# Kernel tuning notes

Measured on AMD Instinct MI355X. Metric: run time of the kernel, lower is better.

## Reference

```python
import jax, jax.numpy as jnp
import numpy as np

B = 2048          # env batch
N = 32            # num_svgd_particles
D = 6             # act_dim
OBS = 17          # obs_dim
H = 256           # q1 hidden width
STEPS = 10        # num_svgd_steps
LR = 0.1          # svgd_lr
LIMIT = 1.0       # act_limit
LOG_NP1 = np.float32(np.log(N + 1.0))


def setup_inputs() -> dict:
    key = jax.random.key(0)
    ks = jax.random.split(key, 6)
    obs = jax.random.normal(ks[0], (B * N, OBS), dtype=jnp.float32)
    a = jax.random.normal(ks[1], (B * N, D), dtype=jnp.float32)
    W1 = jax.random.normal(ks[2], (OBS + D, H), dtype=jnp.float32) / np.float32(np.sqrt(OBS + D))
    b1 = jnp.zeros((H,), dtype=jnp.float32)
    W2 = jax.random.normal(ks[3], (H, H), dtype=jnp.float32) / np.float32(np.sqrt(H))
    b2 = jnp.zeros((H,), dtype=jnp.float32)
    W3 = jax.random.normal(ks[4], (H, 1), dtype=jnp.float32) / np.float32(np.sqrt(H))
    b3 = jnp.zeros((1,), dtype=jnp.float32)
    return {"obs": obs, "a": a, "W1": W1, "b1": b1, "W2": W2, "b2": b2, "W3": W3, "b3": b3}


def q1(obs, X, W1, b1, W2, b2, W3, b3):
    # standard SAC critic: Q(s, a) = MLP(concat(s, a))
    h = jax.nn.relu(jnp.concatenate([obs, X], axis=-1) @ W1 + b1)
    h = jax.nn.relu(h @ W2 + b2)
    return (h @ W3 + b3).squeeze(-1)


def rbf(X):
    # X: (B, N, D); input_2 = X.detach() in the original
    Xd = jax.lax.stop_gradient(X)
    diff = X[:, :, None, :] - Xd[:, None, :, :]          # (B, N, N, D)
    dist_sq = jnp.sum(diff * diff, axis=-1)              # (B, N, N)
    nn = N * N
    # torch.median returns the LOWER of the two middle values for even counts
    med = jnp.sort(jax.lax.stop_gradient(dist_sq).reshape(-1, nn), axis=1)[:, (nn - 1) // 2]
    h = med / (2.0 * LOG_NP1)                            # bandwidth^2 (sigma^2 = h)
    gamma = 1.0 / (1e-8 + 2.0 * h)                       # (B,)
    gamma = gamma[:, None, None]                         # (B, 1, 1)
    kappa = jnp.exp(-gamma * dist_sq)                    # (B, N, N)
    kappa_grad = -2.0 * (diff * gamma[..., None]) * kappa[..., None]  # (B, N, N, D)
    return kappa, diff, gamma, kappa_grad


def reference(obs, a, W1, b1, W2, b2, W3, b3):
    score_fn = jax.grad(lambda Xf: q1(obs, Xf, W1, b1, W2, b2, W3, b3).sum())
    logp = jnp.zeros((B, N), dtype=jnp.float32)

    for _ in range(STEPS):
        score = score_fn(a)                              # (B*N, D)
        X = a.reshape(B, N, D)
        s = score.reshape(B, N, D)
        K_XX, K_diff, K_gamma, K_grad = rbf(X)
        Kd = jax.lax.stop_gradient(K_XX)
        phi = (jnp.einsum('bij,bjd->bid', Kd, s) - K_grad.sum(axis=2)) / N  # (B, N, D)
        line_4 = (K_grad * s[:, None, :, :]).sum(-1).mean(-1)               # (B, N)
        line_5 = -2.0 * K_gamma[:, :, 0] * (
            (-K_grad * K_diff).sum(-1) - D * K_XX
        ).mean(-1)                                                          # (B, N)
        logp = logp - LR * (line_4 + line_5)
        a = jnp.clip(a + LR * phi.reshape(B * N, D), -LIMIT, LIMIT)
        a = jax.lax.stop_gradient(a)

    return a, logp
```

## Files before the change

### kernel.cpp

```cpp
#include <hip/hip_runtime.h>
#include <hip/hip_bf16.h>

#define NB 2048
#define NP 32
#define ND 6
#define NOBS 17
#define NH 256
#define NSTEPS 10
#define C_LR 0.1f
#define C_LIM 1.0f
#define C_LOGNP1 3.4965075614664802f

typedef __bf16 bf16x8 __attribute__((ext_vector_type(8)));
typedef float  f32x4  __attribute__((ext_vector_type(4)));

#define MFMA(a, b, c) __builtin_amdgcn_mfma_f32_16x16x32_bf16(a, b, c, 0, 0, 0)

static __device__ __forceinline__ unsigned short f2bf(float f) {
    union { float f; unsigned u; } c; c.f = f;
    const unsigned r = c.u + 0x7fffu + ((c.u >> 16) & 1u);
    return (unsigned short)(r >> 16);
}

static __device__ __forceinline__ int colpf(int n) {
    return ((n >> 5) << 11) + (((n >> 3) & 3) << 7) + (n & 7);
}

__global__ void prep_swizzle(const float* __restrict__ W1, const float* __restrict__ W2,
                             unsigned short* __restrict__ ws) {
    const int g = blockIdx.x * 256 + threadIdx.x;
    unsigned short v[8];
    if (g < 8192) {
        const int l = g & 63, fid = g >> 6;
        const int kt = fid >> 4, nt = fid & 15;
        const int row0 = kt * 32 + (l >> 4) * 8;
        const int col  = nt * 16 + (l & 15);
#pragma unroll
        for (int j = 0; j < 8; ++j) v[j] = f2bf(W2[(row0 + j) * NH + col]);
        ushort4* dst = (ushort4*)(ws + (size_t)g * 8);
        dst[0] = make_ushort4(v[0], v[1], v[2], v[3]);
        dst[1] = make_ushort4(v[4], v[5], v[6], v[7]);
    } else if (g < 16384) {
        const int e = g - 8192;
        const int l = e & 63, fid = e >> 6;
        const int kt = fid >> 4, nt = fid & 15;
        const int row  = nt * 16 + (l & 15);
        const int col0 = kt * 32 + (l >> 4) * 8;
#pragma unroll
        for (int j = 0; j < 8; ++j) v[j] = f2bf(W2[row * NH + col0 + j]);
        ushort4* dst = (ushort4*)(ws + 65536 + (size_t)e * 8);
        dst[0] = make_ushort4(v[0], v[1], v[2], v[3]);
        dst[1] = make_ushort4(v[4], v[5], v[6], v[7]);
    } else if (g < 16896) {
        const int e = g - 16384;
        const int l = e & 63, kt = e >> 6;
        const int n  = l & 15;
        const int k0 = kt * 32 + (l >> 4) * 8;
#pragma unroll
        for (int j = 0; j < 8; ++j)
            v[j] = (n < ND) ? f2bf(W1[(NOBS + n) * NH + k0 + j]) : (unsigned short)0;
        ushort4* dst = (ushort4*)(ws + 131072 + (size_t)e * 8);
        dst[0] = make_ushort4(v[0], v[1], v[2], v[3]);
        dst[1] = make_ushort4(v[4], v[5], v[6], v[7]);
    } else if (g < 17920) {
        const int e = g - 16896;
        const int l = e & 63, nt = e >> 6;
        const int col = nt * 16 + (l & 15);
        const int r0  = (l >> 4) * 8;
#pragma unroll
        for (int j = 0; j < 8; ++j)
            v[j] = (r0 + j < NOBS + ND) ? f2bf(W1[(r0 + j) * NH + col]) : (unsigned short)0;
        ushort4* dst = (ushort4*)(ws + 135168 + (size_t)e * 8);
        dst[0] = make_ushort4(v[0], v[1], v[2], v[3]);
        dst[1] = make_ushort4(v[4], v[5], v[6], v[7]);
    }
}

__global__ __launch_bounds__(256, 4)
void svgd_kernel(const float* __restrict__ obs, const float* __restrict__ a_in,
                 const float* __restrict__ W1, const float* __restrict__ b1,
                 const float* __restrict__ W2, const float* __restrict__ b2,
                 const float* __restrict__ W3, const unsigned short* __restrict__ ws,
                 float* __restrict__ out)
{
    __shared__ __attribute__((aligned(16))) unsigned short hA[64 * NH];
    __shared__ float Xs[2][384];
    __shared__ float sc_[512];
    __shared__ float med_s[2];

    const int t    = threadIdx.x;
    const int bb   = blockIdx.x;
    const int lane = t & 63;
    const int wid  = t >> 6;
    const int w4   = wid * 4;
    const int quad = lane >> 4;
    const int ln15 = lane & 15;
    const int qo = t >> 7, iao = (t & 127) >> 2, jgo = t & 3;

    const unsigned short* gW2f = ws;
    const unsigned short* gW2b = ws + 65536;
    const unsigned short* gW1p = ws + 131072;
    const unsigned short* gW1f = ws + 135168;

    {
        float* scr = (float*)hA;
        const float* obs_g = obs + (size_t)bb * 1088;
        for (int p = t; p < 1088; p += 256) scr[p] = obs_g[p];
        const float* a_g = a_in + (size_t)bb * 384;
        for (int p = t; p < 384; p += 256) Xs[0][p] = a_g[p];
    }
    __syncthreads();
    bf16x8 a0[4];
    {
        const float* scr = (const float*)hA;
#pragma unroll
        for (int m = 0; m < 4; ++m) {
            const int s = m * 16 + ln15;
#pragma unroll
            for (int j = 0; j < 8; ++j) {
                const int k = quad * 8 + j;
                float v = 0.0f;
                if (k < NOBS) v = scr[s * NOBS + k];
                else if (k < NOBS + ND) v = Xs[0][s * 6 + (k - NOBS)];
                a0[m][j] = (__bf16)v;
            }
        }
    }
    __syncthreads();

    float b1r[4], b2r[4]; unsigned short w3u[4];
#pragma unroll
    for (int q = 0; q < 4; ++q) {
        const int n = (w4 + q) * 16 + ln15;
        b1r[q] = b1[n]; b2r[q] = b2[n]; w3u[q] = f2bf(W3[n]);
    }

    float logp_r = 0.0f;
    int cur = 0;
    const f32x4 zv = {0.f, 0.f, 0.f, 0.f};

    for (int step = 0; step < NSTEPS; ++step) {
        unsigned long long mask1 = 0ull;
        {
            bf16x8 w1B[4];
#pragma unroll
            for (int q = 0; q < 4; ++q)
                w1B[q] = *(const bf16x8*)(gW1f + ((w4 + q) * 64 + lane) * 8);
            f32x4 acc0[4][4];
#pragma unroll
            for (int m = 0; m < 4; ++m)
#pragma unroll
                for (int q = 0; q < 4; ++q) acc0[m][q] = MFMA(a0[m], w1B[q], zv);
#pragma unroll
            for (int q = 0; q < 4; ++q) {
                const int cp = colpf((w4 + q) * 16 + ln15);
#pragma unroll
                for (int m = 0; m < 4; ++m)
#pragma unroll
                    for (int reg = 0; reg < 4; ++reg) {
                        const float hv = acc0[m][q][reg] + b1r[q];
                        const int idx = cp + m * 512 + (quad * 4 + reg) * 8;
                        if (hv > 0.f) {
                            mask1 |= 1ull << (q * 16 + m * 4 + reg);
                            hA[idx] = f2bf(hv);
                        } else hA[idx] = 0;
                    }
            }
        }
        __syncthreads();

        {
            f32x4 acc[4][4];
#pragma unroll
            for (int m = 0; m < 4; ++m)
#pragma unroll
                for (int q = 0; q < 4; ++q) acc[m][q] = zv;
#pragma unroll 2
            for (int kt = 0; kt < 8; ++kt) {
                bf16x8 a[4];
#pragma unroll
                for (int m = 0; m < 4; ++m)
                    a[m] = *(const bf16x8*)&hA[(kt * 4 + m) * 512 + lane * 8];
#pragma unroll
                for (int q = 0; q < 4; ++q) {
                    const bf16x8 bf = *(const bf16x8*)(gW2f + ((kt * 16 + w4 + q) * 64 + lane) * 8);
#pragma unroll
                    for (int m = 0; m < 4; ++m) acc[m][q] = MFMA(a[m], bf, acc[m][q]);
                }
            }
            __syncthreads();
#pragma unroll
            for (int q = 0; q < 4; ++q) {
                const int cp = colpf((w4 + q) * 16 + ln15);
                const float b2v = b2r[q];
                const unsigned short w3v = w3u[q];
#pragma unroll
                for (int m = 0; m < 4; ++m)
#pragma unroll
                    for (int reg = 0; reg < 4; ++reg) {
                        const int idx = cp + m * 512 + (quad * 4 + reg) * 8;
                        hA[idx] = (acc[m][q][reg] + b2v > 0.f) ? w3v : (unsigned short)0;
                    }
            }
        }
        __syncthreads();

        {
            f32x4 acc2[4][4];
#pragma unroll
            for (int m = 0; m < 4; ++m)
#pragma unroll
                for (int q = 0; q < 4; ++q) acc2[m][q] = zv;
#pragma unroll 2
            for (int kt = 0; kt < 8; ++kt) {
                bf16x8 a[4];
#pragma unroll
                for (int m = 0; m < 4; ++m)
                    a[m] = *(const bf16x8*)&hA[(kt * 4 + m) * 512 + lane * 8];
#pragma unroll
                for (int q = 0; q < 4; ++q) {
                    const bf16x8 bf = *(const bf16x8*)(gW2b + ((kt * 16 + w4 + q) * 64 + lane) * 8);
#pragma unroll
                    for (int m = 0; m < 4; ++m) acc2[m][q] = MFMA(a[m], bf, acc2[m][q]);
                }
            }
            __syncthreads();
#pragma unroll
            for (int q = 0; q < 4; ++q) {
                const int cp = colpf((w4 + q) * 16 + ln15);
#pragma unroll
                for (int m = 0; m < 4; ++m)
#pragma unroll
                    for (int reg = 0; reg < 4; ++reg) {
                        const int idx = cp + m * 512 + (quad * 4 + reg) * 8;
                        hA[idx] = ((mask1 >> (q * 16 + m * 4 + reg)) & 1ull)
                                      ? f2bf(acc2[m][q][reg]) : (unsigned short)0;
                    }
            }
        }
        __syncthreads();

        if (wid >= 2) {
            const int mb = (wid - 2) * 2;
            f32x4 sa[2] = {zv, zv};
#pragma unroll
            for (int kt = 0; kt < 8; ++kt) {
                const bf16x8 bw = *(const bf16x8*)(gW1p + (kt * 64 + lane) * 8);
#pragma unroll
                for (int mm = 0; mm < 2; ++mm) {
                    const bf16x8 a = *(const bf16x8*)&hA[(kt * 4 + mb + mm) * 512 + lane * 8];
                    sa[mm] = MFMA(a, bw, sa[mm]);
                }
            }
            if (ln15 < ND) {
#pragma unroll
                for (int mm = 0; mm < 2; ++mm)
#pragma unroll
                    for (int reg = 0; reg < 4; ++reg)
                        sc_[((mb + mm) * 16 + quad * 4 + reg) * 8 + ln15] = sa[mm][reg];
            }
        } else {
            const float* Xc = &Xs[cur][wid * 192];
            unsigned u[8];
#pragma unroll
            for (int r = 0; r < 8; ++r) {
                const int e = lane + 64 * r;
                if (e < 496) {
                    int i = (int)((63.0f - sqrtf(3969.0f - 8.0f * (float)e)) * 0.5f);
                    while (i * (63 - i) / 2 > e) --i;
                    while ((i + 1) * (62 - i) / 2 <= e) ++i;
                    const int j = i + 1 + (e - i * (63 - i) / 2);
                    float s = 0.f;
#pragma unroll
                    for (int d = 0; d < ND; ++d) {
                        const float df = Xc[i * 6 + d] - Xc[j * 6 + d];
                        s += df * df;
                    }
                    u[r] = __float_as_uint(s);
                } else u[r] = 0x7f800000u;
            }
            unsigned P = 0u;
            for (int bit = 30; bit >= 0; --bit) {
                const unsigned Q = P | (1u << bit);
                int c = 0;
#pragma unroll
                for (int r = 0; r < 8; ++r)
                    c += __popcll(__ballot(u[r] < Q));
                if (c <= 239) P = Q;
            }
            if (lane == 0) med_s[wid] = __uint_as_float(P);
        }
        __syncthreads();

        {
            const int nxt = cur ^ 1;
            const float gam = 1.0f / (1e-8f + med_s[qo] / C_LOGNP1);
            const float* Xc = &Xs[cur][qo * 192];
            float xi[6];
#pragma unroll
            for (int d = 0; d < ND; ++d) xi[d] = Xc[iao * 6 + d];
            float w[8] = {0, 0, 0, 0, 0, 0, 0, 0};
#pragma unroll
            for (int jj = 0; jj < 8; ++jj) {
                const int j = jgo * 8 + jj;
                float df6[6], sj6[6];
                float dsv = 0.f, dot = 0.f;
#pragma unroll
                for (int d = 0; d < ND; ++d) {
                    df6[d] = xi[d] - Xc[j * 6 + d];
                    sj6[d] = sc_[(qo * 32 + j) * 8 + d];
                    dsv += df6[d] * df6[d];
                    dot += df6[d] * sj6[d];
                }
                const float kap = __expf(-gam * dsv);
                const float tg = 2.0f * gam * kap;
#pragma unroll
                for (int d = 0; d < ND; ++d) w[d] += kap * sj6[d] + tg * df6[d];
                w[6] -= tg * dot;
                w[7] += tg * dsv - 6.0f * kap;
            }
#pragma unroll
            for (int off = 1; off < 4; off <<= 1)
#pragma unroll
                for (int c = 0; c < 8; ++c) w[c] += __shfl_xor(w[c], off);
            const int base = (qo * 32 + iao) * 6;
            {
                float x = xi[jgo] + C_LR * (w[jgo] * (1.0f / 32.0f));
                Xs[nxt][base + jgo] = fminf(fmaxf(x, -C_LIM), C_LIM);
            }
            if (jgo < 2) {
                const int d = jgo + 4;
                float x = xi[d] + C_LR * (w[d] * (1.0f / 32.0f));
                Xs[nxt][base + d] = fminf(fmaxf(x, -C_LIM), C_LIM);
            }
            if (jgo == 3)
                logp_r -= C_LR * (w[6] * (1.0f / 32.0f)
                                  - 2.0f * gam * (w[7] * (1.0f / 32.0f)));
        }
        __syncthreads();

        cur ^= 1;
        if (quad == 2) {
#pragma unroll
            for (int m = 0; m < 4; ++m) {
                const int s = m * 16 + ln15;
#pragma unroll
                for (int j = 1; j <= 6; ++j)
                    a0[m][j] = (__bf16)Xs[cur][s * 6 + (j - 1)];
            }
        }
    }

    for (int p = t; p < 384; p += 256) out[(size_t)bb * 384 + p] = Xs[cur][p];
    if (jgo == 3) out[(size_t)NB * NP * ND + bb * 64 + qo * 32 + iao] = logp_r;
}

extern "C" void kernel_launch(void* const* d_in, const int* in_sizes, int n_in,
                              void* d_out, int out_size, void* d_ws, size_t ws_size,
                              hipStream_t stream) {
    const float* obs = (const float*)d_in[0];
    const float* a   = (const float*)d_in[1];
    const float* W1  = (const float*)d_in[2];
    const float* b1  = (const float*)d_in[3];
    const float* W2  = (const float*)d_in[4];
    const float* b2  = (const float*)d_in[5];
    const float* W3  = (const float*)d_in[6];
    unsigned short* wsu = (unsigned short*)d_ws;
    float* out = (float*)d_out;

    prep_swizzle<<<70, 256, 0, stream>>>(W1, W2, wsu);
    svgd_kernel<<<NB / 2, 256, 0, stream>>>(obs, a, W1, b1, W2, b2, W3, wsu, out);
}
```

Baseline: 488.5 us.

## Re-swizzle hidden LDS layout, fold biases into MFMA, pack bf16 conversions, stagger block start

```diff
diff --git a/kernel.cpp b/kernel.cpp
--- a/kernel.cpp
+++ b/kernel.cpp
@@ -22,8 +22,14 @@
     return (unsigned short)(r >> 16);
 }
 
-static __device__ __forceinline__ int colpf(int n) {
-    return ((n >> 5) << 11) + (((n >> 3) & 3) << 7) + (n & 7);
+static __device__ __forceinline__ unsigned pk2bf(float a, float b) {
+#if __has_builtin(__builtin_amdgcn_cvt_pk_bf16_f32)
+    auto p = __builtin_amdgcn_cvt_pk_bf16_f32(a, b);
+    unsigned u; __builtin_memcpy(&u, &p, 4);
+    return u;
+#else
+    return (unsigned)f2bf(a) | ((unsigned)f2bf(b) << 16);
+#endif
 }
 
 __global__ void prep_swizzle(const float* __restrict__ W1, const float* __restrict__ W2,
@@ -97,10 +103,25 @@
     const int ln15 = lane & 15;
     const int qo = t >> 7, iao = (t & 127) >> 2, jgo = t & 3;
 
+    {
+        const int slot = (bb >> 8) & 3;
+        for (int i = 0; i < slot * 20; ++i) __builtin_amdgcn_s_sleep(8);
+    }
+
     const unsigned short* gW2f = ws;
     const unsigned short* gW2b = ws + 65536;
     const unsigned short* gW1p = ws + 131072;
     const unsigned short* gW1f = ws + 135168;
+
+    const int aoff = (lane & 3) * 128 + (lane >> 5) * 64
+                   + ((lane >> 2) & 3) * 16 + ((lane >> 4) & 1) * 8;
+    int kqb[4];
+#pragma unroll
+    for (int q = 0; q < 4; ++q) {
+        const int nt = w4 + q;
+        kqb[q] = (nt >> 1) * 2048 + (nt & 1) * 64 + quad * 16
+               + (ln15 >> 3) * 8 + (ln15 & 7);
+    }
 
     {
         float* scr = (float*)hA;
@@ -140,7 +161,7 @@
     const f32x4 zv = {0.f, 0.f, 0.f, 0.f};
 
     for (int step = 0; step < NSTEPS; ++step) {
-        unsigned long long mask1 = 0ull;
+        unsigned msk[2] = {0u, 0u};
         {
             bf16x8 w1B[4];
 #pragma unroll
@@ -150,21 +171,27 @@
 #pragma unroll
             for (int m = 0; m < 4; ++m)
 #pragma unroll
-                for (int q = 0; q < 4; ++q) acc0[m][q] = MFMA(a0[m], w1B[q], zv);
+                for (int q = 0; q < 4; ++q) {
+                    const f32x4 cb = {b1r[q], b1r[q], b1r[q], b1r[q]};
+                    acc0[m][q] = MFMA(a0[m], w1B[q], cb);
+                }
 #pragma unroll
             for (int q = 0; q < 4; ++q) {
-                const int cp = colpf((w4 + q) * 16 + ln15);
-#pragma unroll
-                for (int m = 0; m < 4; ++m)
-#pragma unroll
-                    for (int reg = 0; reg < 4; ++reg) {
-                        const float hv = acc0[m][q][reg] + b1r[q];
-                        const int idx = cp + m * 512 + (quad * 4 + reg) * 8;
-                        if (hv > 0.f) {
-                            mask1 |= 1ull << (q * 16 + m * 4 + reg);
-                            hA[idx] = f2bf(hv);
-                        } else hA[idx] = 0;
-                    }
+                const int kq = kqb[q];
+#pragma unroll
+                for (int m = 0; m < 4; ++m) {
+                    const f32x4 v = acc0[m][q];
+                    const unsigned p01 = pk2bf(fmaxf(v[0], 0.f), fmaxf(v[1], 0.f));
+                    const unsigned p23 = pk2bf(fmaxf(v[2], 0.f), fmaxf(v[3], 0.f));
+                    unsigned short* bp = &hA[kq + m * 512];
+                    bp[0]   = (unsigned short)p01;
+                    bp[128] = (unsigned short)(p01 >> 16);
+                    bp[256] = (unsigned short)p23;
+                    bp[384] = (unsigned short)(p23 >> 16);
+                    const unsigned mm = (v[0] > 0.f ? 1u : 0u) | (v[1] > 0.f ? 2u : 0u)
+                                      | (v[2] > 0.f ? 4u : 0u) | (v[3] > 0.f ? 8u : 0u);
+                    msk[q >> 1] |= mm << ((q & 1) * 16 + m * 4);
+                }
             }
         }
         __syncthreads();
@@ -174,13 +201,16 @@
 #pragma unroll
             for (int m = 0; m < 4; ++m)
 #pragma unroll
-                for (int q = 0; q < 4; ++q) acc[m][q] = zv;
+                for (int q = 0; q < 4; ++q) {
+                    const f32x4 cb = {b2r[q], b2r[q], b2r[q], b2r[q]};
+                    acc[m][q] = cb;
+                }
 #pragma unroll 2
             for (int kt = 0; kt < 8; ++kt) {
                 bf16x8 a[4];
 #pragma unroll
                 for (int m = 0; m < 4; ++m)
-                    a[m] = *(const bf16x8*)&hA[(kt * 4 + m) * 512 + lane * 8];
+                    a[m] = *(const bf16x8*)&hA[(kt * 4 + m) * 512 + aoff];
 #pragma unroll
                 for (int q = 0; q < 4; ++q) {
                     const bf16x8 bf = *(const bf16x8*)(gW2f + ((kt * 16 + w4 + q) * 64 + lane) * 8);
@@ -191,16 +221,17 @@
             __syncthreads();
 #pragma unroll
             for (int q = 0; q < 4; ++q) {
-                const int cp = colpf((w4 + q) * 16 + ln15);
-                const float b2v = b2r[q];
+                const int kq = kqb[q];
                 const unsigned short w3v = w3u[q];
 #pragma unroll
-                for (int m = 0; m < 4; ++m)
-#pragma unroll
-                    for (int reg = 0; reg < 4; ++reg) {
-                        const int idx = cp + m * 512 + (quad * 4 + reg) * 8;
-                        hA[idx] = (acc[m][q][reg] + b2v > 0.f) ? w3v : (unsigned short)0;
-                    }
+                for (int m = 0; m < 4; ++m) {
+                    const f32x4 v = acc[m][q];
+                    unsigned short* bp = &hA[kq + m * 512];
+                    bp[0]   = v[0] > 0.f ? w3v : (unsigned short)0;
+                    bp[128] = v[1] > 0.f ? w3v : (unsigned short)0;
+                    bp[256] = v[2] > 0.f ? w3v : (unsigned short)0;
+                    bp[384] = v[3] > 0.f ? w3v : (unsigned short)0;
+                }
             }
         }
         __syncthreads();
@@ -216,7 +247,7 @@
                 bf16x8 a[4];
 #pragma unroll
                 for (int m = 0; m < 4; ++m)
-                    a[m] = *(const bf16x8*)&hA[(kt * 4 + m) * 512 + lane * 8];
+                    a[m] = *(const bf16x8*)&hA[(kt * 4 + m) * 512 + aoff];
 #pragma unroll
                 for (int q = 0; q < 4; ++q) {
                     const bf16x8 bf = *(const bf16x8*)(gW2b + ((kt * 16 + w4 + q) * 64 + lane) * 8);
@@ -227,15 +258,24 @@
             __syncthreads();
 #pragma unroll
             for (int q = 0; q < 4; ++q) {
-                const int cp = colpf((w4 + q) * 16 + ln15);
-#pragma unroll
-                for (int m = 0; m < 4; ++m)
-#pragma unroll
-                    for (int reg = 0; reg < 4; ++reg) {
-                        const int idx = cp + m * 512 + (quad * 4 + reg) * 8;
-                        hA[idx] = ((mask1 >> (q * 16 + m * 4 + reg)) & 1ull)
-                                      ? f2bf(acc2[m][q][reg]) : (unsigned short)0;
-                    }
+                const int kq = kqb[q];
+                const unsigned ma = msk[q >> 1];
+#pragma unroll
+                for (int m = 0; m < 4; ++m) {
+                    const f32x4 v = acc2[m][q];
+                    const int b0 = (q & 1) * 16 + m * 4;
+                    const float t0 = (ma & (1u << (b0 + 0))) ? v[0] : 0.f;
+                    const float t1 = (ma & (1u << (b0 + 1))) ? v[1] : 0.f;
+                    const float t2 = (ma & (1u << (b0 + 2))) ? v[2] : 0.f;
+                    const float t3 = (ma & (1u << (b0 + 3))) ? v[3] : 0.f;
+                    const unsigned p01 = pk2bf(t0, t1);
+                    const unsigned p23 = pk2bf(t2, t3);
+                    unsigned short* bp = &hA[kq + m * 512];
+                    bp[0]   = (unsigned short)p01;
+                    bp[128] = (unsigned short)(p01 >> 16);
+                    bp[256] = (unsigned short)p23;
+                    bp[384] = (unsigned short)(p23 >> 16);
+                }
             }
         }
         __syncthreads();
@@ -248,7 +288,7 @@
                 const bf16x8 bw = *(const bf16x8*)(gW1p + (kt * 64 + lane) * 8);
 #pragma unroll
                 for (int mm = 0; mm < 2; ++mm) {
-                    const bf16x8 a = *(const bf16x8*)&hA[(kt * 4 + mb + mm) * 512 + lane * 8];
+                    const bf16x8 a = *(const bf16x8*)&hA[(kt * 4 + mb + mm) * 512 + aoff];
                     sa[mm] = MFMA(a, bw, sa[mm]);
                 }
             }
```

Result: slower. 634.5 us (+29.9%).
